# Kernel optimization log

Measured on AMD Instinct MI355X. Metric: run time of the kernel, lower is better.

## Reference

```python
import jax, jax.numpy as jnp
import numpy as np

B, L, F, H = 16, 4096, 512, 512


def setup_inputs() -> dict:
    key = jax.random.key(0)
    ks = jax.random.split(key, 8)
    return {
        "x": jax.random.normal(ks[0], (B, L, F), dtype=jnp.float32),
        "B_real": jax.random.normal(ks[1], (F, H), dtype=jnp.float32),
        "B_img": jax.random.normal(ks[2], (F, H), dtype=jnp.float32),
        "nu": jax.random.normal(ks[3], (H,), dtype=jnp.float32),
        "theta": jax.random.uniform(ks[4], (H,), dtype=jnp.float32),
        "delta": jax.random.uniform(ks[5], (H,), dtype=jnp.float32),
        "h0_real": jax.random.normal(ks[6], (H,), dtype=jnp.float32),
        "h0_img": jax.random.normal(ks[7], (H,), dtype=jnp.float32),
    }


def reference(x, B_real, B_img, nu, theta, delta, h0_real, h0_img):
    # Diagonal complex recurrence: h_t = lam * h_{t-1} + delta * (B x_t),
    # h_0 = h0_real + i h0_img, returning Re(h_1..h_L).
    lam = jnp.exp(-jnp.exp(nu) + 1j * theta)  # (H,) complex64
    # Input projection (compute-bound GEMMs), then scale by delta.
    Bx = (jnp.matmul(x, B_real) + 1j * jnp.matmul(x, B_img)) * delta  # (B,L,H)

    bsz, seqlen, hid = Bx.shape
    lam_b = jnp.broadcast_to(lam, Bx.shape)

    def combine(e1, e2):
        a1, b1 = e1
        a2, b2 = e2
        return (a1 * a2, a2 * b1 + b2)

    # Log-depth associative scan over the sequence axis (equiv. to the
    # torch Blelchon-style doubling loop; front zero-padding is a no-op).
    _, h = jax.lax.associative_scan(combine, (lam_b, Bx), axis=1)

    # h0 contribution: lam^{t+1} * h0 for t = 0..L-1
    lam_pow = jnp.cumprod(jnp.broadcast_to(lam, (seqlen, hid)), axis=0)  # (L,H)
    h0 = h0_real + 1j * h0_img  # (H,)
    h0_contrib = lam_pow[None, :, :] * h0[None, None, :]  # (1,L,H)
    return (h + h0_contrib).real
```

## Files before the change

### kernel.cpp

```cpp
#include <hip/hip_runtime.h>

typedef __attribute__((ext_vector_type(8))) short s16x8;
typedef __attribute__((ext_vector_type(4))) float f32x4;

constexpr int B_ = 16;
constexpr int L_ = 4096;
constexpr int F_ = 512;
constexpr int H_ = 512;
constexpr int CT = 32;
constexpr int NC = L_ / CT;
constexpr int KC = 16;
constexpr int XROW = 520;

constexpr size_t WSOUT_OFF   = (size_t)9 << 20;
constexpr size_t WSOUT_BYTES = (size_t)B_ * L_ * H_ * 2;

static __device__ __forceinline__ unsigned short f2bf(float f) {
  union { float f; unsigned u; } v; v.f = f;
  unsigned r = (v.u + 0x7FFFu + ((v.u >> 16) & 1u)) >> 16;
  return (unsigned short)r;
}
static __device__ __forceinline__ float bf2f(unsigned short s) {
  union { unsigned u; float f; } v; v.u = ((unsigned)s) << 16;
  return v.f;
}

__global__ void bprep_kernel(const float* __restrict__ BR, const float* __restrict__ BI,
                             s16x8* __restrict__ BpR, s16x8* __restrict__ BpI) {
  int ht = blockIdx.x >> 4;
  int fk = blockIdx.x & 15;
  int l  = threadIdx.x;
  int h  = ht * 16 + (l & 15);
  int f0 = fk * 32 + (l >> 4) * 8;
  s16x8 r, im;
#pragma unroll
  for (int j = 0; j < 8; ++j) {
    r[j]  = (short)f2bf(BR[(size_t)(f0 + j) * H_ + h]);
    im[j] = (short)f2bf(BI[(size_t)(f0 + j) * H_ + h]);
  }
  int idx = (ht * 16 + fk) * 64 + l;
  BpR[idx] = r;
  BpI[idx] = im;
}

template <bool FUSED>
__global__ __launch_bounds__(512, 1) void gemm_scan_kernel(
    const float* __restrict__ x,
    const s16x8* __restrict__ BpR, const s16x8* __restrict__ BpI,
    const float* __restrict__ nu, const float* __restrict__ theta,
    const float* __restrict__ delta,
    float* __restrict__ out, unsigned short* __restrict__ wsout,
    float* __restrict__ ER, float* __restrict__ EI) {
  __shared__ __align__(16) unsigned short xs[CT * XROW];

  const int ls   = blockIdx.x;
  const int hq   = blockIdx.y;
  const int b    = blockIdx.z;
  const int tid  = threadIdx.x;
  const int lane = tid & 63;
  const int w    = tid >> 6;
  const int g    = lane >> 4;
  const int cl   = lane & 15;

  const int ht = hq * 8 + w;
  const int h  = ht * 16 + cl;

  s16x8 Brg[16], Big[16];
#pragma unroll
  for (int fk = 0; fk < 16; ++fk) {
    Brg[fk] = BpR[(ht * 16 + fk) * 64 + lane];
    Big[fk] = BpI[(ht * 16 + fk) * 64 + lane];
  }

  const float dl = delta[h];
  const float mag = __expf(-__expf(nu[h]));
  const float thv = theta[h];
  const float lr = mag * __cosf(thv), li = mag * __sinf(thv);
  const float l2r = lr*lr - li*li,     l2i = 2.f*lr*li;
  const float l3r = l2r*lr - l2i*li,   l3i = l2r*li + l2i*lr;
  const float l4r = l2r*l2r - l2i*l2i, l4i = 2.f*l2r*l2i;
  const float l8r = l4r*l4r - l4i*l4i, l8i = 2.f*l4r*l4i;
  const float l12r = l8r*l4r - l8i*l4i, l12i = l8r*l4i + l8i*l4r;
  const float l16r = l8r*l8r - l8i*l8i, l16i = 2.f*l8r*l8i;
  const float m4r = (g==0)?1.f:((g==1)?l4r:((g==2)?l8r:l12r));
  const float m4i = (g==0)?0.f:((g==1)?l4i:((g==2)?l8i:l12i));

  const float* xbase = x + (size_t)(b * L_ + ls * KC * CT) * F_;

  float4 pv[4][2];
#pragma unroll
  for (int i = 0; i < 4; ++i) {
    int row = i * 8 + w;
    pv[i][0] = *(const float4*)(xbase + (size_t)row * F_ + lane * 8);
    pv[i][1] = *(const float4*)(xbase + (size_t)row * F_ + lane * 8 + 4);
  }

#pragma unroll 1
  for (int k = 0; k < KC; ++k) {
    __syncthreads();

#pragma unroll
    for (int i = 0; i < 4; ++i) {
      int row = i * 8 + w;
      s16x8 pk;
      pk[0] = (short)f2bf(pv[i][0].x); pk[1] = (short)f2bf(pv[i][0].y);
      pk[2] = (short)f2bf(pv[i][0].z); pk[3] = (short)f2bf(pv[i][0].w);
      pk[4] = (short)f2bf(pv[i][1].x); pk[5] = (short)f2bf(pv[i][1].y);
      pk[6] = (short)f2bf(pv[i][1].z); pk[7] = (short)f2bf(pv[i][1].w);
      *(s16x8*)(&xs[row * XROW + lane * 8]) = pk;
    }
    __syncthreads();

    if (k + 1 < KC) {
      const float* xq = xbase + (size_t)(k + 1) * CT * F_;
#pragma unroll
      for (int i = 0; i < 4; ++i) {
        int row = i * 8 + w;
        pv[i][0] = *(const float4*)(xq + (size_t)row * F_ + lane * 8);
        pv[i][1] = *(const float4*)(xq + (size_t)row * F_ + lane * 8 + 4);
      }
    }

    f32x4 accR[2], accI[2];
#pragma unroll
    for (int tt = 0; tt < 2; ++tt) {
      accR[tt] = (f32x4){0.f, 0.f, 0.f, 0.f};
      accI[tt] = (f32x4){0.f, 0.f, 0.f, 0.f};
    }
    __builtin_amdgcn_s_setprio(1);
#pragma unroll
    for (int fk = 0; fk < 16; ++fk) {
      s16x8 a[2];
#pragma unroll
      for (int tt = 0; tt < 2; ++tt)
        a[tt] = *(const s16x8*)(&xs[(tt * 16 + cl) * XROW + fk * 32 + g * 8]);
#pragma unroll
      for (int tt = 0; tt < 2; ++tt) {
        accR[tt] = __builtin_amdgcn_mfma_f32_16x16x32_bf16(a[tt], Brg[fk], accR[tt], 0, 0, 0);
        accI[tt] = __builtin_amdgcn_mfma_f32_16x16x32_bf16(a[tt], Big[fk], accI[tt], 0, 0, 0);
      }
    }
    __builtin_amdgcn_s_setprio(0);

    const int c = ls * KC + k;
    {
      float carryR = 0.f, carryI = 0.f;
      float* opf = out + (size_t)(b * L_ + c * CT) * H_ + h;
      unsigned short* opw = FUSED ? (wsout + (size_t)(b * L_ + c * CT) * H_ + h) : nullptr;

#pragma unroll
      for (int tt = 0; tt < 2; ++tt) {
        float lsR[4], lsI[4];
        float sR = 0.f, sI = 0.f;
#pragma unroll
        for (int r = 0; r < 4; ++r) {
          float uR = dl * accR[tt][r], uI = dl * accI[tt][r];
          float nR = lr * sR - li * sI + uR;
          float nI = lr * sI + li * sR + uI;
          sR = nR; sI = nI; lsR[r] = sR; lsI[r] = sI;
        }
        float qR = __shfl(sR, (lane - 16) & 63, 64);
        float qI = __shfl(sI, (lane - 16) & 63, 64);
        float I1R = (g >= 1) ? sR + l4r*qR - l4i*qI : sR;
        float I1I = (g >= 1) ? sI + l4r*qI + l4i*qR : sI;
        float q2R = __shfl(I1R, (lane - 32) & 63, 64);
        float q2I = __shfl(I1I, (lane - 32) & 63, 64);
        float I2R = (g >= 2) ? I1R + l8r*q2R - l8i*q2I : I1R;
        float I2I = (g >= 2) ? I1I + l8r*q2I + l8i*q2R : I1I;
        float eR = __shfl(I2R, (lane - 16) & 63, 64);
        float eI = __shfl(I2I, (lane - 16) & 63, 64);
        eR = (g >= 1) ? eR : 0.f;
        eI = (g >= 1) ? eI : 0.f;
        float incR = m4r * carryR - m4i * carryI + eR;
        float incI = m4r * carryI + m4i * carryR + eI;
        {
          float o0 = lsR[0] + lr  * incR - li  * incI;
          float o1 = lsR[1] + l2r * incR - l2i * incI;
          float o2 = lsR[2] + l3r * incR - l3i * incI;
          float o3 = lsR[3] + l4r * incR - l4i * incI;
          if (FUSED) {
            opw[(size_t)(tt * 16 + g * 4 + 0) * H_] = f2bf(o0);
            opw[(size_t)(tt * 16 + g * 4 + 1) * H_] = f2bf(o1);
            opw[(size_t)(tt * 16 + g * 4 + 2) * H_] = f2bf(o2);
            opw[(size_t)(tt * 16 + g * 4 + 3) * H_] = f2bf(o3);
          } else {
            opf[(size_t)(tt * 16 + g * 4 + 0) * H_] = o0;
            opf[(size_t)(tt * 16 + g * 4 + 1) * H_] = o1;
            opf[(size_t)(tt * 16 + g * 4 + 2) * H_] = o2;
            opf[(size_t)(tt * 16 + g * 4 + 3) * H_] = o3;
          }
        }
        float fR = __shfl(I2R, 48 | cl, 64);
        float fI = __shfl(I2I, 48 | cl, 64);
        float ncR = fR + l16r * carryR - l16i * carryI;
        float ncI = fI + l16r * carryI + l16i * carryR;
        carryR = ncR; carryI = ncI;
      }
      if (g == 0) {
        size_t eidx = (size_t)(b * NC + c) * H_ + h;
        ER[eidx] = carryR;
        EI[eidx] = carryI;
      }
    }
  }
}

__global__ void combine_kernel(const float* __restrict__ nu, const float* __restrict__ theta,
                               const float* __restrict__ h0r, const float* __restrict__ h0i,
                               float* __restrict__ ER, float* __restrict__ EI) {
  int gg = blockIdx.x * blockDim.x + threadIdx.x;
  int b = gg >> 9;
  int h = gg & (H_ - 1);
  float mag = __expf(-__expf(nu[h]));
  float lr  = mag * __cosf(theta[h]);
  float li  = mag * __sinf(theta[h]);
  float pr = lr, pi = li;
#pragma unroll
  for (int s = 0; s < 5; ++s) {
    float nr = pr * pr - pi * pi;
    float ni = 2.f * pr * pi;
    pr = nr; pi = ni;
  }
  float sR = h0r[h], sI = h0i[h];
  for (int c0 = 0; c0 < NC; c0 += 8) {
    float tR[8], tI[8];
#pragma unroll
    for (int k = 0; k < 8; ++k) {
      size_t idx = (size_t)(b * NC + c0 + k) * H_ + h;
      tR[k] = ER[idx]; tI[k] = EI[idx];
    }
#pragma unroll
    for (int k = 0; k < 8; ++k) {
      size_t idx = (size_t)(b * NC + c0 + k) * H_ + h;
      ER[idx] = sR; EI[idx] = sI;
      float nR = pr * sR - pi * sI + tR[k];
      float nI = pr * sI + pi * sR + tI[k];
      sR = nR; sI = nI;
    }
  }
}

__global__ void fixup_kernel(const float* __restrict__ nu, const float* __restrict__ theta,
                             const float* __restrict__ ER, const float* __restrict__ EI,
                             float* __restrict__ out) {
  int c = blockIdx.x, b = blockIdx.y;
  int h = threadIdx.x;
  size_t idx = (size_t)(b * NC + c) * H_ + h;
  float hR = ER[idx], hI = EI[idx];
  float mag = __expf(-__expf(nu[h]));
  float lr  = mag * __cosf(theta[h]);
  float li  = mag * __sinf(theta[h]);
  float pr = lr, pi = li;
  float* op = out + (size_t)(b * L_ + c * CT) * H_ + h;
#pragma unroll 4
  for (int k = 0; k < CT; ++k) {
    op[(size_t)k * H_] += pr * hR - pi * hI;
    float nr = pr * lr - pi * li;
    float ni = pr * li + pi * lr;
    pr = nr; pi = ni;
  }
}

__global__ void fixup_fused_kernel(const float* __restrict__ nu, const float* __restrict__ theta,
                                   const float* __restrict__ ER, const float* __restrict__ EI,
                                   const unsigned short* __restrict__ wsout,
                                   float* __restrict__ out) {
  int c = blockIdx.x, b = blockIdx.y;
  int h = threadIdx.x;
  size_t idx = (size_t)(b * NC + c) * H_ + h;
  float hR = ER[idx], hI = EI[idx];
  float mag = __expf(-__expf(nu[h]));
  float lr  = mag * __cosf(theta[h]);
  float li  = mag * __sinf(theta[h]);
  float pr = lr, pi = li;
  size_t base = (size_t)(b * L_ + c * CT) * H_ + h;
  const unsigned short* wp = wsout + base;
  float* op = out + base;
#pragma unroll 4
  for (int k = 0; k < CT; ++k) {
    op[(size_t)k * H_] = bf2f(wp[(size_t)k * H_]) + (pr * hR - pi * hI);
    float nr = pr * lr - pi * li;
    float ni = pr * li + pi * lr;
    pr = nr; pi = ni;
  }
}

extern "C" void kernel_launch(void* const* d_in, const int* in_sizes, int n_in,
                              void* d_out, int out_size, void* d_ws, size_t ws_size,
                              hipStream_t stream) {
  const float* x   = (const float*)d_in[0];
  const float* BR  = (const float*)d_in[1];
  const float* BI  = (const float*)d_in[2];
  const float* nu  = (const float*)d_in[3];
  const float* th  = (const float*)d_in[4];
  const float* dl  = (const float*)d_in[5];
  const float* h0r = (const float*)d_in[6];
  const float* h0i = (const float*)d_in[7];
  float* out = (float*)d_out;

  char* wsc = (char*)d_ws;
  s16x8* BpR = (s16x8*)(wsc);
  s16x8* BpI = (s16x8*)(wsc + (512 << 10));
  float* ER  = (float*)(wsc + (1 << 20));
  float* EI  = (float*)(wsc + (1 << 20) + (size_t)B_ * NC * H_ * 4);
  unsigned short* wsout = (unsigned short*)(wsc + WSOUT_OFF);
  const bool fused = ws_size >= WSOUT_OFF + WSOUT_BYTES;

  hipLaunchKernelGGL(bprep_kernel, dim3(512), dim3(64), 0, stream, BR, BI, BpR, BpI);
  if (fused) {
    hipLaunchKernelGGL((gemm_scan_kernel<true>), dim3(8, 4, B_), dim3(512), 0, stream,
                       x, BpR, BpI, nu, th, dl, out, wsout, ER, EI);
    hipLaunchKernelGGL(combine_kernel, dim3(16), dim3(512), 0, stream, nu, th, h0r, h0i, ER, EI);
    hipLaunchKernelGGL(fixup_fused_kernel, dim3(NC, B_), dim3(512), 0, stream,
                       nu, th, ER, EI, wsout, out);
  } else {
    hipLaunchKernelGGL((gemm_scan_kernel<false>), dim3(8, 4, B_), dim3(512), 0, stream,
                       x, BpR, BpI, nu, th, dl, out, wsout, ER, EI);
    hipLaunchKernelGGL(combine_kernel, dim3(16), dim3(512), 0, stream, nu, th, h0r, h0i, ER, EI);
    hipLaunchKernelGGL(fixup_kernel, dim3(NC, B_), dim3(512), 0, stream, nu, th, ER, EI, out);
  }
}
```

Before: 157.2 us.

## Double-buffer LDS tiles and overlap chunk scan with next chunk's MFMA

Shared-memory staging of the x tile is double-buffered, and the loop is software-pipelined so the MFMA for chunk k runs alongside the complex scan and output stores of chunk k-1. This drops one barrier per iteration and lets matrix-core work overlap with the shuffle-heavy scan and global stores. In exchange it doubles the LDS tile footprint and keeps two sets of accumulators live, which adds register pressure in a kernel that already holds the full B fragments in registers.

```diff
diff --git a/kernel.cpp b/kernel.cpp
--- a/kernel.cpp
+++ b/kernel.cpp
@@ -51,7 +51,7 @@
     const float* __restrict__ delta,
     float* __restrict__ out, unsigned short* __restrict__ wsout,
     float* __restrict__ ER, float* __restrict__ EI) {
-  __shared__ __align__(16) unsigned short xs[CT * XROW];
+  __shared__ __align__(16) unsigned short xs[2][CT * XROW];
 
   const int ls   = blockIdx.x;
   const int hq   = blockIdx.y;
@@ -87,122 +87,141 @@
 
   const float* xbase = x + (size_t)(b * L_ + ls * KC * CT) * F_;
 
-  float4 pv[4][2];
-#pragma unroll
-  for (int i = 0; i < 4; ++i) {
-    int row = i * 8 + w;
-    pv[i][0] = *(const float4*)(xbase + (size_t)row * F_ + lane * 8);
-    pv[i][1] = *(const float4*)(xbase + (size_t)row * F_ + lane * 8 + 4);
-  }
-
-#pragma unroll 1
-  for (int k = 0; k < KC; ++k) {
-    __syncthreads();
-
+  auto do_scan = [&](const f32x4* aR, const f32x4* aI, int c) {
+    float carryR = 0.f, carryI = 0.f;
+    float* opf = out + (size_t)(b * L_ + c * CT) * H_ + h;
+    unsigned short* opw = FUSED ? (wsout + (size_t)(b * L_ + c * CT) * H_ + h) : nullptr;
+
+#pragma unroll
+    for (int tt = 0; tt < 2; ++tt) {
+      float lsR[4], lsI[4];
+      float sR = 0.f, sI = 0.f;
+#pragma unroll
+      for (int r = 0; r < 4; ++r) {
+        float uR = dl * aR[tt][r], uI = dl * aI[tt][r];
+        float nR = lr * sR - li * sI + uR;
+        float nI = lr * sI + li * sR + uI;
+        sR = nR; sI = nI; lsR[r] = sR; lsI[r] = sI;
+      }
+      float qR = __shfl(sR, (lane - 16) & 63, 64);
+      float qI = __shfl(sI, (lane - 16) & 63, 64);
+      float I1R = (g >= 1) ? sR + l4r*qR - l4i*qI : sR;
+      float I1I = (g >= 1) ? sI + l4r*qI + l4i*qR : sI;
+      float q2R = __shfl(I1R, (lane - 32) & 63, 64);
+      float q2I = __shfl(I1I, (lane - 32) & 63, 64);
+      float I2R = (g >= 2) ? I1R + l8r*q2R - l8i*q2I : I1R;
+      float I2I = (g >= 2) ? I1I + l8r*q2I + l8i*q2R : I1I;
+      float eR = __shfl(I2R, (lane - 16) & 63, 64);
+      float eI = __shfl(I2I, (lane - 16) & 63, 64);
+      eR = (g >= 1) ? eR : 0.f;
+      eI = (g >= 1) ? eI : 0.f;
+      float incR = m4r * carryR - m4i * carryI + eR;
+      float incI = m4r * carryI + m4i * carryR + eI;
+      {
+        float o0 = lsR[0] + lr  * incR - li  * incI;
+        float o1 = lsR[1] + l2r * incR - l2i * incI;
+        float o2 = lsR[2] + l3r * incR - l3i * incI;
+        float o3 = lsR[3] + l4r * incR - l4i * incI;
+        if (FUSED) {
+          opw[(size_t)(tt * 16 + g * 4 + 0) * H_] = f2bf(o0);
+          opw[(size_t)(tt * 16 + g * 4 + 1) * H_] = f2bf(o1);
+          opw[(size_t)(tt * 16 + g * 4 + 2) * H_] = f2bf(o2);
+          opw[(size_t)(tt * 16 + g * 4 + 3) * H_] = f2bf(o3);
+        } else {
+          opf[(size_t)(tt * 16 + g * 4 + 0) * H_] = o0;
+          opf[(size_t)(tt * 16 + g * 4 + 1) * H_] = o1;
+          opf[(size_t)(tt * 16 + g * 4 + 2) * H_] = o2;
+          opf[(size_t)(tt * 16 + g * 4 + 3) * H_] = o3;
+        }
+      }
+      float fR = __shfl(I2R, 48 | cl, 64);
+      float fI = __shfl(I2I, 48 | cl, 64);
+      float ncR = fR + l16r * carryR - l16i * carryI;
+      float ncI = fI + l16r * carryI + l16i * carryR;
+      carryR = ncR; carryI = ncI;
+    }
+    if (g == 0) {
+      size_t eidx = (size_t)(b * NC + c) * H_ + h;
+      ER[eidx] = carryR;
+      EI[eidx] = carryI;
+    }
+  };
+
+  auto do_mfma = [&](int bi, f32x4* aR, f32x4* aI) {
+#pragma unroll
+    for (int tt = 0; tt < 2; ++tt) {
+      aR[tt] = (f32x4){0.f, 0.f, 0.f, 0.f};
+      aI[tt] = (f32x4){0.f, 0.f, 0.f, 0.f};
+    }
+    __builtin_amdgcn_s_setprio(1);
+#pragma unroll
+    for (int fk = 0; fk < 16; ++fk) {
+      s16x8 a[2];
+#pragma unroll
+      for (int tt = 0; tt < 2; ++tt)
+        a[tt] = *(const s16x8*)(&xs[bi][(tt * 16 + cl) * XROW + fk * 32 + g * 8]);
+#pragma unroll
+      for (int tt = 0; tt < 2; ++tt) {
+        aR[tt] = __builtin_amdgcn_mfma_f32_16x16x32_bf16(a[tt], Brg[fk], aR[tt], 0, 0, 0);
+        aI[tt] = __builtin_amdgcn_mfma_f32_16x16x32_bf16(a[tt], Big[fk], aI[tt], 0, 0, 0);
+      }
+    }
+    __builtin_amdgcn_s_setprio(0);
+  };
+
+  auto stage_write = [&](int bi, const float4 p[4][2]) {
 #pragma unroll
     for (int i = 0; i < 4; ++i) {
       int row = i * 8 + w;
       s16x8 pk;
-      pk[0] = (short)f2bf(pv[i][0].x); pk[1] = (short)f2bf(pv[i][0].y);
-      pk[2] = (short)f2bf(pv[i][0].z); pk[3] = (short)f2bf(pv[i][0].w);
-      pk[4] = (short)f2bf(pv[i][1].x); pk[5] = (short)f2bf(pv[i][1].y);
-      pk[6] = (short)f2bf(pv[i][1].z); pk[7] = (short)f2bf(pv[i][1].w);
-      *(s16x8*)(&xs[row * XROW + lane * 8]) = pk;
-    }
+      pk[0] = (short)f2bf(p[i][0].x); pk[1] = (short)f2bf(p[i][0].y);
+      pk[2] = (short)f2bf(p[i][0].z); pk[3] = (short)f2bf(p[i][0].w);
+      pk[4] = (short)f2bf(p[i][1].x); pk[5] = (short)f2bf(p[i][1].y);
+      pk[6] = (short)f2bf(p[i][1].z); pk[7] = (short)f2bf(p[i][1].w);
+      *(s16x8*)(&xs[bi][row * XROW + lane * 8]) = pk;
+    }
+  };
+  auto stage_load = [&](int k, float4 p[4][2]) {
+    const float* xq = xbase + (size_t)k * CT * F_;
+#pragma unroll
+    for (int i = 0; i < 4; ++i) {
+      int row = i * 8 + w;
+      p[i][0] = *(const float4*)(xq + (size_t)row * F_ + lane * 8);
+      p[i][1] = *(const float4*)(xq + (size_t)row * F_ + lane * 8 + 4);
+    }
+  };
+
+  f32x4 accOldR[2], accOldI[2], accNewR[2], accNewI[2];
+
+  {
+    float4 p0[4][2];
+    stage_load(0, p0);
+    stage_write(0, p0);
+  }
+  __syncthreads();
+  {
+    float4 pv[4][2];
+    stage_load(1, pv);
+    do_mfma(0, accOldR, accOldI);
+    stage_write(1, pv);
+  }
+  __syncthreads();
+
+#pragma unroll 1
+  for (int k = 1; k < KC; ++k) {
+    float4 pv[4][2];
+    if (k + 1 < KC) stage_load(k + 1, pv);
+    do_mfma(k & 1, accNewR, accNewI);
+    do_scan(accOldR, accOldI, ls * KC + (k - 1));
+    if (k + 1 < KC) stage_write((k + 1) & 1, pv);
     __syncthreads();
-
-    if (k + 1 < KC) {
-      const float* xq = xbase + (size_t)(k + 1) * CT * F_;
-#pragma unroll
-      for (int i = 0; i < 4; ++i) {
-        int row = i * 8 + w;
-        pv[i][0] = *(const float4*)(xq + (size_t)row * F_ + lane * 8);
-        pv[i][1] = *(const float4*)(xq + (size_t)row * F_ + lane * 8 + 4);
-      }
-    }
-
-    f32x4 accR[2], accI[2];
 #pragma unroll
     for (int tt = 0; tt < 2; ++tt) {
-      accR[tt] = (f32x4){0.f, 0.f, 0.f, 0.f};
-      accI[tt] = (f32x4){0.f, 0.f, 0.f, 0.f};
-    }
-    __builtin_amdgcn_s_setprio(1);
-#pragma unroll
-    for (int fk = 0; fk < 16; ++fk) {
-      s16x8 a[2];
-#pragma unroll
-      for (int tt = 0; tt < 2; ++tt)
-        a[tt] = *(const s16x8*)(&xs[(tt * 16 + cl) * XROW + fk * 32 + g * 8]);
-#pragma unroll
-      for (int tt = 0; tt < 2; ++tt) {
-        accR[tt] = __builtin_amdgcn_mfma_f32_16x16x32_bf16(a[tt], Brg[fk], accR[tt], 0, 0, 0);
-        accI[tt] = __builtin_amdgcn_mfma_f32_16x16x32_bf16(a[tt], Big[fk], accI[tt], 0, 0, 0);
-      }
-    }
-    __builtin_amdgcn_s_setprio(0);
-
-    const int c = ls * KC + k;
-    {
-      float carryR = 0.f, carryI = 0.f;
-      float* opf = out + (size_t)(b * L_ + c * CT) * H_ + h;
-      unsigned short* opw = FUSED ? (wsout + (size_t)(b * L_ + c * CT) * H_ + h) : nullptr;
-
-#pragma unroll
-      for (int tt = 0; tt < 2; ++tt) {
-        float lsR[4], lsI[4];
-        float sR = 0.f, sI = 0.f;
-#pragma unroll
-        for (int r = 0; r < 4; ++r) {
-          float uR = dl * accR[tt][r], uI = dl * accI[tt][r];
-          float nR = lr * sR - li * sI + uR;
-          float nI = lr * sI + li * sR + uI;
-          sR = nR; sI = nI; lsR[r] = sR; lsI[r] = sI;
-        }
-        float qR = __shfl(sR, (lane - 16) & 63, 64);
-        float qI = __shfl(sI, (lane - 16) & 63, 64);
-        float I1R = (g >= 1) ? sR + l4r*qR - l4i*qI : sR;
-        float I1I = (g >= 1) ? sI + l4r*qI + l4i*qR : sI;
-        float q2R = __shfl(I1R, (lane - 32) & 63, 64);
-        float q2I = __shfl(I1I, (lane - 32) & 63, 64);
-        float I2R = (g >= 2) ? I1R + l8r*q2R - l8i*q2I : I1R;
-        float I2I = (g >= 2) ? I1I + l8r*q2I + l8i*q2R : I1I;
-        float eR = __shfl(I2R, (lane - 16) & 63, 64);
-        float eI = __shfl(I2I, (lane - 16) & 63, 64);
-        eR = (g >= 1) ? eR : 0.f;
-        eI = (g >= 1) ? eI : 0.f;
-        float incR = m4r * carryR - m4i * carryI + eR;
-        float incI = m4r * carryI + m4i * carryR + eI;
-        {
-          float o0 = lsR[0] + lr  * incR - li  * incI;
-          float o1 = lsR[1] + l2r * incR - l2i * incI;
-          float o2 = lsR[2] + l3r * incR - l3i * incI;
-          float o3 = lsR[3] + l4r * incR - l4i * incI;
-          if (FUSED) {
-            opw[(size_t)(tt * 16 + g * 4 + 0) * H_] = f2bf(o0);
-            opw[(size_t)(tt * 16 + g * 4 + 1) * H_] = f2bf(o1);
-            opw[(size_t)(tt * 16 + g * 4 + 2) * H_] = f2bf(o2);
-            opw[(size_t)(tt * 16 + g * 4 + 3) * H_] = f2bf(o3);
-          } else {
-            opf[(size_t)(tt * 16 + g * 4 + 0) * H_] = o0;
-            opf[(size_t)(tt * 16 + g * 4 + 1) * H_] = o1;
-            opf[(size_t)(tt * 16 + g * 4 + 2) * H_] = o2;
-            opf[(size_t)(tt * 16 + g * 4 + 3) * H_] = o3;
-          }
-        }
-        float fR = __shfl(I2R, 48 | cl, 64);
-        float fI = __shfl(I2I, 48 | cl, 64);
-        float ncR = fR + l16r * carryR - l16i * carryI;
-        float ncI = fI + l16r * carryI + l16i * carryR;
-        carryR = ncR; carryI = ncI;
-      }
-      if (g == 0) {
-        size_t eidx = (size_t)(b * NC + c) * H_ + h;
-        ER[eidx] = carryR;
-        EI[eidx] = carryI;
-      }
-    }
-  }
+      accOldR[tt] = accNewR[tt];
+      accOldI[tt] = accNewI[tt];
+    }
+  }
+  do_scan(accOldR, accOldI, ls * KC + (KC - 1));
 }
 
 __global__ void combine_kernel(const float* __restrict__ nu, const float* __restrict__ theta,
```

After: 163.3 us. 3.9% more time.
